# Kernel tuning notes

Measured on AMD Instinct MI355X. Metric: run time of the kernel, lower is better.

The kernel has to match this reference:

```python
import jax, jax.numpy as jnp
import numpy as np

ITER_STEPS = 2
NODE_DIM = 512

def _rmv(t, m, value):
    # allennlp.replace_masked_values: keep t where mask nonzero, else value
    return jnp.where(m != 0, t, value)

def setup_inputs() -> dict:
    key = jax.random.key(0)
    ks = jax.random.split(key, 24)
    B, R, C, D, d = 16, 64, 64, 2048, NODE_DIM
    inp = {
        "question_node": jax.random.normal(ks[0], (B, d), jnp.float32),
        "table_row_header_nodes": jax.random.normal(ks[1], (B, R, d), jnp.float32),
        "table_col_header_nodes": jax.random.normal(ks[2], (B, C, d), jnp.float32),
        "table_data_cell_nodes": jax.random.normal(ks[3], (B, D, d), jnp.float32),
        "table_row_header_index_mask": jax.random.randint(ks[4], (B, R), 0, 2, jnp.int32),
        "table_col_header_index_mask": jax.random.randint(ks[5], (B, C), 0, 2, jnp.int32),
        "table_data_cell_index_mask": jax.random.randint(ks[6], (B, D), 0, 2, jnp.int32),
        "same_row_data_cell_relation": jax.random.randint(ks[7], (B, D, D), 0, 2, jnp.int32),
        "same_col_data_cell_relation": jax.random.randint(ks[8], (B, D, D), 0, 2, jnp.int32),
        "data_cell_row_rel": jax.random.randint(ks[9], (B, R, D), 0, 2, jnp.int32),
        "data_cell_col_rel": jax.random.randint(ks[10], (B, C, D), 0, 2, jnp.int32),
        # parameters (Linear(in,out) stores weight [out,in]; y = x @ W.T)
        "w_node": jax.random.normal(ks[11], (1, d), jnp.float32) / np.sqrt(d),
        "w_row_data_cell": jax.random.normal(ks[12], (d, d), jnp.float32) / np.sqrt(d),
        "w_col_data_cell": jax.random.normal(ks[13], (d, d), jnp.float32) / np.sqrt(d),
        "w_data_cell_row": jax.random.normal(ks[14], (d, d), jnp.float32) / np.sqrt(d),
        "w_data_cell_col": jax.random.normal(ks[15], (d, d), jnp.float32) / np.sqrt(d),
        "w_same_row": jax.random.normal(ks[16], (d, d), jnp.float32) / np.sqrt(d),
        "w_same_col": jax.random.normal(ks[17], (d, d), jnp.float32) / np.sqrt(d),
        "w_row_question": jax.random.normal(ks[18], (d, d), jnp.float32) / np.sqrt(d),
        "w_col_question": jax.random.normal(ks[19], (d, d), jnp.float32) / np.sqrt(d),
    }
    return inp


def reference(question_node, table_row_header_nodes, table_col_header_nodes,
              table_data_cell_nodes, table_row_header_index_mask,
              table_col_header_index_mask, table_data_cell_index_mask,
              same_row_data_cell_relation, same_col_data_cell_relation,
              data_cell_row_rel, data_cell_col_rel,
              w_node, w_row_data_cell, w_col_data_cell, w_data_cell_row,
              w_data_cell_col, w_same_row, w_same_col, w_row_question,
              w_col_question):
    rm = table_row_header_index_mask.astype(jnp.float32)   # [B,R]
    cm = table_col_header_index_mask.astype(jnp.float32)   # [B,C]
    dm = table_data_cell_index_mask.astype(jnp.float32)    # [B,D]

    # masked relation graphs (0/1 float)
    rh_dc_graph = data_cell_row_rel.astype(jnp.float32) * (rm[:, :, None] * dm[:, None, :])   # [B,R,D]
    ch_dc_graph = data_cell_col_rel.astype(jnp.float32) * (cm[:, :, None] * dm[:, None, :])   # [B,C,D]
    dc_dc_mask = dm[:, :, None] * dm[:, None, :]
    same_row_graph = same_row_data_cell_relation.astype(jnp.float32) * dc_dc_mask             # [B,D,D]
    same_col_graph = same_col_data_cell_relation.astype(jnp.float32) * dc_dc_mask             # [B,D,D]

    rh_num = rh_dc_graph.sum(-1)                                  # [B,R]
    rh_num = _rmv(rh_num + 1.0, (rh_num >= 1), 1.0)
    ch_num = ch_dc_graph.sum(-1)                                  # [B,C]
    ch_num = _rmv(ch_num + 1.0, (ch_num >= 1), 1.0)
    dc_num = (same_row_graph.sum(-1) + same_col_graph.sum(-1)
              + rh_dc_graph.sum(1) + ch_dc_graph.sum(1))          # [B,D]
    dc_num = _rmv(dc_num, (dc_num >= 1), 1.0)

    rh = table_row_header_nodes
    ch = table_col_header_nodes
    dc = table_data_cell_nodes
    q = question_node

    for _ in range(ITER_STEPS):
        rh_w = jax.nn.sigmoid(rh @ w_node.T)[..., 0]   # [B,R]
        ch_w = jax.nn.sigmoid(ch @ w_node.T)[..., 0]   # [B,C]
        dc_w = jax.nn.sigmoid(dc @ w_node.T)[..., 0]   # [B,D]

        rh_dc_info = dc @ w_row_data_cell.T            # [B,D,d]
        ch_dc_info = dc @ w_col_data_cell.T            # [B,D,d]
        rh_q_info = (q @ w_row_question.T)[:, None, :] * rm[:, :, None]  # [B,R,d]
        ch_q_info = (q @ w_col_question.T)[:, None, :] * cm[:, :, None]  # [B,C,d]
        same_row_info = dc @ w_same_row.T              # [B,D,d]
        same_col_info = dc @ w_same_col.T              # [B,D,d]
        dc_rh_info = rh @ w_data_cell_row.T            # [B,R,d]
        dc_ch_info = ch @ w_data_cell_col.T            # [B,C,d]

        # gated adjacency weights: source-node sigmoid gate masked by graph
        rh_dc_weight = jnp.where(rh_dc_graph != 0, dc_w[:, None, :], 0.0)         # [B,R,D]
        ch_dc_weight = jnp.where(ch_dc_graph != 0, dc_w[:, None, :], 0.0)         # [B,C,D]
        same_row_weight = jnp.where(same_row_graph != 0, dc_w[:, None, :], 0.0)   # [B,D,D]
        same_col_weight = jnp.where(same_col_graph != 0, dc_w[:, None, :], 0.0)   # [B,D,D]
        dc_rh_weight = jnp.where(jnp.swapaxes(rh_dc_graph, 1, 2) != 0, rh_w[:, None, :], 0.0)  # [B,D,R]
        dc_ch_weight = jnp.where(jnp.swapaxes(ch_dc_graph, 1, 2) != 0, ch_w[:, None, :], 0.0)  # [B,D,C]

        rh_dc_agg = jnp.matmul(rh_dc_weight, rh_dc_info)        # [B,R,d]
        ch_dc_agg = jnp.matmul(ch_dc_weight, ch_dc_info)        # [B,C,d]
        same_row_agg = jnp.matmul(same_row_weight, same_row_info)  # [B,D,d]
        same_col_agg = jnp.matmul(same_col_weight, same_col_info)  # [B,D,d]
        dc_rh_agg = jnp.matmul(dc_rh_weight, dc_rh_info)        # [B,D,d]
        dc_ch_agg = jnp.matmul(dc_ch_weight, dc_ch_info)        # [B,D,d]

        agg_rh = (rh_dc_agg + rh_q_info) / rh_num[:, :, None]
        agg_ch = (ch_dc_agg + ch_q_info) / ch_num[:, :, None]
        # NOTE: faithful to source bug: dc_ch_agg appears twice, same_col_agg unused
        agg_dc = (same_row_agg + dc_ch_agg + dc_rh_agg + dc_ch_agg) / dc_num[:, :, None]

        rh = jax.nn.relu(agg_rh)
        ch = jax.nn.relu(agg_ch)
        dc = jax.nn.relu(agg_dc)

    return (rh, ch, dc)
```

## Files before the change

kernel.cpp:

```cpp
#include <hip/hip_runtime.h>
#include <math.h>

#define NB 16
#define NR 64
#define NCOL 64
#define ND 2048
#define DIM 512

typedef __attribute__((ext_vector_type(4))) float f32x4;
typedef __attribute__((ext_vector_type(8))) short bf16x8;
typedef __attribute__((ext_vector_type(8))) unsigned short us8;

#define OFF_RHNUM  0L
#define OFF_CHNUM  1024L
#define OFF_DCNUM  2048L
#define OFF_RHW    34816L
#define OFF_CHW    35840L
#define OFF_QROW   36864L
#define OFF_QCOL   45056L
#define OFF_PRER   53248L
#define OFF_PREC   577536L
#define OFF_INFORC 1101824L
#define OFF_BITS   2150400L
#define OFF_DCS    4247552L
#define OFF_PROJ   21024768L
#define WS_FLOATS  37801984L

__device__ inline void bsplit(float v, unsigned short& h, unsigned short& l) {
    unsigned uv = __float_as_uint(v);
    unsigned hb = (uv + 0x7FFFu + ((uv >> 16) & 1u)) >> 16;
    h = (unsigned short)hb;
    float lo = v - __uint_as_float(hb << 16);
    unsigned lv = __float_as_uint(lo);
    l = (unsigned short)((lv + 0x7FFFu + ((lv >> 16) & 1u)) >> 16);
}

__device__ inline unsigned spread4(unsigned x) {
    x = (x | (x << 12)) & 0x000F000Fu;
    x = (x | (x << 6))  & 0x03030303u;
    x = (x | (x << 3))  & 0x11111111u;
    return x;
}

__global__ __launch_bounds__(256) void k_gate_rc(
    const float* __restrict__ rh, const float* __restrict__ ch,
    const int* __restrict__ rm, const int* __restrict__ cm,
    const float* __restrict__ wnode,
    float* __restrict__ rh_w, float* __restrict__ ch_w)
{
    int wave = threadIdx.x >> 6, lane = threadIdx.x & 63;
    int idx = blockIdx.x * 4 + wave;
    const float* xrow; float* outw; int mval;
    if (idx < NB * NR) {
        int b = idx >> 6, r = idx & 63;
        xrow = rh + ((long)b * NR + r) * DIM; mval = rm[b * NR + r]; outw = rh_w + b * NR + r;
    } else {
        int tt = idx - NB * NR; int b = tt >> 6, c = tt & 63;
        xrow = ch + ((long)b * NCOL + c) * DIM; mval = cm[b * NCOL + c]; outw = ch_w + b * NCOL + c;
    }
    const float4* px = (const float4*)xrow;
    const float4* pw = (const float4*)wnode;
    float4 xa = px[lane * 2], xb = px[lane * 2 + 1];
    float4 wa = pw[lane * 2], wb = pw[lane * 2 + 1];
    float s = xa.x * wa.x + xa.y * wa.y + xa.z * wa.z + xa.w * wa.w
            + xb.x * wb.x + xb.y * wb.y + xb.z * wb.z + xb.w * wb.w;
    #pragma unroll
    for (int o = 32; o > 0; o >>= 1) s += __shfl_xor(s, o, 64);
    if (lane == 0) {
        float g = 1.f / (1.f + expf(-s));
        *outw = mval ? g : 0.f;
    }
}

__global__ __launch_bounds__(256) void k_split(
    const float* __restrict__ src, const float* __restrict__ wnode, const int* __restrict__ dmask,
    unsigned short* __restrict__ dhi, unsigned short* __restrict__ dlo,
    unsigned short* __restrict__ thi, unsigned short* __restrict__ tlo)
{
    int b = blockIdx.y, j0 = blockIdx.x * 16;
    __shared__ float X[16 * 512];
    __shared__ float scs[16];
    int t = threadIdx.x;
    int r = t >> 4, u = t & 15;
    const float* row = src + ((long)b * ND + j0 + r) * DIM;
    float part = 0.f;
    #pragma unroll
    for (int i = 0; i < 8; i++) {
        int col = i * 64 + u * 4;
        float4 v = *(const float4*)(row + col);
        float4 w = *(const float4*)(wnode + col);
        part += v.x * w.x + v.y * w.y + v.z * w.z + v.w * w.w;
        *(float4*)&X[r * 512 + (col ^ ((r & 7) * 4))] = v;
    }
    part += __shfl_xor(part, 1, 64);
    part += __shfl_xor(part, 2, 64);
    part += __shfl_xor(part, 4, 64);
    part += __shfl_xor(part, 8, 64);
    if (u == 0) {
        float g = 1.f / (1.f + expf(-part));
        scs[r] = (dmask[(long)b * ND + j0 + r] != 0) ? g : 0.f;
    }
    __syncthreads();
    {
        float s = scs[r];
        long ob = ((long)b * ND + j0 + r) * DIM + u * 32;
        #pragma unroll
        for (int g = 0; g < 4; g++) {
            us8 ph, pl;
            #pragma unroll
            for (int e = 0; e < 8; e++) {
                int cc = u * 32 + g * 8 + e;
                float v = X[r * 512 + (cc ^ ((r & 7) * 4))] * s;
                unsigned short hh, ll; bsplit(v, hh, ll);
                ph[e] = hh; pl[e] = ll;
            }
            *(us8*)(dhi + ob + g * 8) = ph;
            *(us8*)(dlo + ob + g * 8) = pl;
        }
    }
    #pragma unroll
    for (int h = 0; h < 2; h++) {
        int n = t + h * 256;
        us8 ph0, ph1, pl0, pl1;
        #pragma unroll
        for (int rr = 0; rr < 16; rr++) {
            float v = X[rr * 512 + (n ^ ((rr & 7) * 4))] * scs[rr];
            unsigned short hh, ll; bsplit(v, hh, ll);
            if (rr < 8) { ph0[rr] = hh; pl0[rr] = ll; }
            else        { ph1[rr - 8] = hh; pl1[rr - 8] = ll; }
        }
        long ob = ((long)b * DIM + n) * ND + j0;
        *(us8*)(thi + ob) = ph0; *(us8*)(thi + ob + 8) = ph1;
        *(us8*)(tlo + ob) = pl0; *(us8*)(tlo + ob + 8) = pl1;
    }
}

__global__ __launch_bounds__(256) void k_wsplit(
    const float* __restrict__ w, unsigned short* __restrict__ whi, unsigned short* __restrict__ wlo)
{
    long i = ((long)blockIdx.x * 256 + threadIdx.x) * 8;
    float4 a = *(const float4*)(w + i), b4 = *(const float4*)(w + i + 4);
    float v[8] = {a.x, a.y, a.z, a.w, b4.x, b4.y, b4.z, b4.w};
    us8 ph, pl;
    #pragma unroll
    for (int t = 0; t < 8; t++) {
        unsigned short hh, ll; bsplit(v[t], hh, ll);
        ph[t] = hh; pl[t] = ll;
    }
    *(us8*)(whi + i) = ph;
    *(us8*)(wlo + i) = pl;
}

__global__ __launch_bounds__(256) void k_q(
    const float* __restrict__ q, const float* __restrict__ wrq, const float* __restrict__ wcq,
    float* __restrict__ qrow, float* __restrict__ qcol)
{
    int b = blockIdx.z;
    const float* W = blockIdx.y ? wcq : wrq;
    float* out = blockIdx.y ? qcol : qrow;
    int wave = threadIdx.x >> 6, lane = threadIdx.x & 63;
    int n = blockIdx.x * 4 + wave;
    const float4* qp = (const float4*)(q + (long)b * DIM);
    const float4* wp = (const float4*)(W + (long)n * DIM);
    float4 a0 = qp[lane * 2], a1 = qp[lane * 2 + 1];
    float4 w0 = wp[lane * 2], w1 = wp[lane * 2 + 1];
    float s = a0.x * w0.x + a0.y * w0.y + a0.z * w0.z + a0.w * w0.w
            + a1.x * w1.x + a1.y * w1.y + a1.z * w1.z + a1.w * w1.w;
    #pragma unroll
    for (int o = 32; o > 0; o >>= 1) s += __shfl_xor(s, o, 64);
    if (lane == 0) out[(long)b * DIM + n] = s;
}

__global__ __launch_bounds__(256) void k_bits(
    const int* __restrict__ sr, const int* __restrict__ sc, const int* __restrict__ dmask,
    unsigned* __restrict__ bits, float* __restrict__ dcnum)
{
    long bi = blockIdx.x;
    int b = (int)(bi >> 11);
    int dmi = dmask[bi];
    int wave = threadIdx.x >> 6, lane = threadIdx.x & 63;
    const int4* sr4 = (const int4*)(sr + bi * ND);
    const int4* sc4 = (const int4*)(sc + bi * ND);
    const int4* dm4 = (const int4*)(dmask + (long)b * ND);
    unsigned* brow = bits + bi * 64;
    int cnt = 0;
    #pragma unroll
    for (int h = 0; h < 2; h++) {
        int vidx = wave * 128 + h * 64 + lane;
        int4 vs = sr4[vidx];
        int4 vc = sc4[vidx];
        int4 vd = dm4[vidx];
        bool d0 = dmi && vd.x, d1 = dmi && vd.y, d2 = dmi && vd.z, d3 = dmi && vd.w;
        unsigned long long m0 = __ballot(d0 && vs.x);
        unsigned long long m1 = __ballot(d1 && vs.y);
        unsigned long long m2 = __ballot(d2 && vs.z);
        unsigned long long m3 = __ballot(d3 && vs.w);
        unsigned long long n0 = __ballot(d0 && vc.x);
        unsigned long long n1 = __ballot(d1 && vc.y);
        unsigned long long n2 = __ballot(d2 && vc.z);
        unsigned long long n3 = __ballot(d3 && vc.w);
        cnt += __popcll(m0) + __popcll(m1) + __popcll(m2) + __popcll(m3)
             + __popcll(n0) + __popcll(n1) + __popcll(n2) + __popcll(n3);
        if (lane < 8) {
            unsigned w = spread4((unsigned)(m0 >> (8 * lane)) & 0xFFu)
                       | (spread4((unsigned)(m1 >> (8 * lane)) & 0xFFu) << 1)
                       | (spread4((unsigned)(m2 >> (8 * lane)) & 0xFFu) << 2)
                       | (spread4((unsigned)(m3 >> (8 * lane)) & 0xFFu) << 3);
            brow[wave * 16 + h * 8 + lane] = w;
        }
    }
    __shared__ int red[4];
    if (lane == 0) red[wave] = cnt;
    __syncthreads();
    if (threadIdx.x == 0) dcnum[bi] = (float)(red[0] + red[1] + red[2] + red[3]);
}

__global__ __launch_bounds__(256) void k_rcnum(
    const int* __restrict__ rel_rd, const int* __restrict__ rel_cd,
    const int* __restrict__ rm, const int* __restrict__ cm, const int* __restrict__ dmask,
    float* __restrict__ rh_num, float* __restrict__ ch_num)
{
    int wave = threadIdx.x >> 6, lane = threadIdx.x & 63;
    long idx = (long)blockIdx.x * 4 + wave;
    const int* row; int mval; float* out; const int* dmb;
    if (idx < NB * NR) {
        int b = (int)(idx >> 6), r = (int)(idx & 63);
        row = rel_rd + ((long)b * NR + r) * ND; mval = rm[b * NR + r];
        out = rh_num + b * NR + r; dmb = dmask + (long)b * ND;
    } else {
        long tt = idx - NB * NR; int b = (int)(tt >> 6), c = (int)(tt & 63);
        row = rel_cd + ((long)b * NCOL + c) * ND; mval = cm[b * NCOL + c];
        out = ch_num + b * NCOL + c; dmb = dmask + (long)b * ND;
    }
    int cnt = 0;
    for (int rr = 0; rr < 32; rr++) {
        int j = rr * 64 + lane;
        cnt += (row[j] != 0 && dmb[j] != 0) ? 1 : 0;
    }
    #pragma unroll
    for (int o = 32; o > 0; o >>= 1) cnt += __shfl_xor(cnt, o, 64);
    if (lane == 0) {
        float s = mval ? (float)cnt : 0.f;
        *out = (s >= 1.f) ? (s + 1.f) : 1.f;
    }
}

__global__ __launch_bounds__(256) void k_dcnum_final(
    const int* __restrict__ rel_rd, const int* __restrict__ rel_cd,
    const int* __restrict__ rm, const int* __restrict__ cm, const int* __restrict__ dmask,
    float* __restrict__ dcnum)
{
    int b = blockIdx.y;
    int j = blockIdx.x * 256 + threadIdx.x;
    const int* rd = rel_rd + (long)b * NR * ND;
    const int* cd = rel_cd + (long)b * NCOL * ND;
    const int* rmb = rm + b * NR;
    const int* cmb = cm + b * NCOL;
    int cnt = 0;
    for (int r = 0; r < NR; r++)  cnt += (rd[(long)r * ND + j] != 0 && rmb[r] != 0) ? 1 : 0;
    for (int c = 0; c < NCOL; c++) cnt += (cd[(long)c * ND + j] != 0 && cmb[c] != 0) ? 1 : 0;
    float add = (dmask[(long)b * ND + j] != 0) ? (float)cnt : 0.f;
    float tv = dcnum[(long)b * ND + j] + add;
    dcnum[(long)b * ND + j] = (tv >= 1.f) ? tv : 1.f;
}

template<int EPI>
__global__ __launch_bounds__(256) void gemm_small(
    const float* __restrict__ A, long sA,
    const float* __restrict__ W,
    float* __restrict__ C, long sC,
    const float* __restrict__ rowscale, float alpha,
    const int* __restrict__ mrow, const float* __restrict__ addvec,
    const float* __restrict__ rownum, int rsb)
{
    int b = blockIdx.z;
    int n0 = blockIdx.x * 64;
    __shared__ float As[32][68], Ws[32][68];
    float acc[4][4] = {};
    int tx = threadIdx.x & 15, ty = threadIdx.x >> 4;
    int lm = threadIdx.x >> 2, lk = (threadIdx.x & 3) * 8;
    const float* Ab = A + (long)b * sA;
    for (int k0 = 0; k0 < DIM; k0 += 32) {
        const float4* pa = (const float4*)(Ab + (long)lm * DIM + k0 + lk);
        float4 va0 = pa[0], va1 = pa[1];
        const float4* pw = (const float4*)(W + (long)(n0 + lm) * DIM + k0 + lk);
        float4 vw0 = pw[0], vw1 = pw[1];
        As[lk + 0][lm] = va0.x; As[lk + 1][lm] = va0.y; As[lk + 2][lm] = va0.z; As[lk + 3][lm] = va0.w;
        As[lk + 4][lm] = va1.x; As[lk + 5][lm] = va1.y; As[lk + 6][lm] = va1.z; As[lk + 7][lm] = va1.w;
        Ws[lk + 0][lm] = vw0.x; Ws[lk + 1][lm] = vw0.y; Ws[lk + 2][lm] = vw0.z; Ws[lk + 3][lm] = vw0.w;
        Ws[lk + 4][lm] = vw1.x; Ws[lk + 5][lm] = vw1.y; Ws[lk + 6][lm] = vw1.z; Ws[lk + 7][lm] = vw1.w;
        __syncthreads();
        #pragma unroll
        for (int kk = 0; kk < 32; kk++) {
            float4 av = *(const float4*)&As[kk][ty * 4];
            float4 wv = *(const float4*)&Ws[kk][tx * 4];
            float a[4] = {av.x, av.y, av.z, av.w};
            float w[4] = {wv.x, wv.y, wv.z, wv.w};
            #pragma unroll
            for (int mi = 0; mi < 4; mi++)
                #pragma unroll
                for (int ni = 0; ni < 4; ni++)
                    acc[mi][ni] += a[mi] * w[ni];
        }
        __syncthreads();
    }
    #pragma unroll
    for (int mi = 0; mi < 4; mi++) {
        int gm = ty * 4 + mi;
        float vals[4];
        if (EPI == 1) {
            float scv = alpha * rowscale[(long)b * rsb + gm];
            #pragma unroll
            for (int ni = 0; ni < 4; ni++) vals[ni] = scv * acc[mi][ni];
        } else {
            float mq = (mrow[(long)b * rsb + gm] != 0) ? 1.f : 0.f;
            float inv = 1.f / rownum[(long)b * rsb + gm];
            #pragma unroll
            for (int ni = 0; ni < 4; ni++) {
                float tv = (acc[mi][ni] + mq * addvec[(long)b * DIM + n0 + tx * 4 + ni]) * inv;
                vals[ni] = fmaxf(tv, 0.f);
            }
        }
        float4 o; o.x = vals[0]; o.y = vals[1]; o.z = vals[2]; o.w = vals[3];
        *(float4*)(C + (long)b * sC + (long)gm * DIM + n0 + tx * 4) = o;
    }
}

__global__ __launch_bounds__(256) void k_pre_rc_mfma(
    const int* __restrict__ rel_rd, const int* __restrict__ rel_cd,
    const unsigned short* __restrict__ thi, const unsigned short* __restrict__ tlo,
    const int* __restrict__ rm, const int* __restrict__ cm,
    float* __restrict__ pre_r, float* __restrict__ pre_c)
{
    int b = blockIdx.y, n0 = blockIdx.x * 64;
    __shared__ unsigned short Aexp[128 * 64];
    __shared__ unsigned short Bhi[64 * 64], Blo[64 * 64];
    int tid = threadIdx.x, lane = tid & 63, wid = tid >> 6;
    int wm = wid >> 1, wn = wid & 1;
    int arow = tid >> 1, aseg = tid & 1;
    const int* relrow = (arow < 64)
        ? rel_rd + ((long)b * 64 + arow) * ND
        : rel_cd + ((long)b * 64 + arow - 64) * ND;
    int bn = tid >> 2, bq = tid & 3;
    const unsigned short* bsrc_h = thi + ((long)b * DIM + n0 + bn) * ND;
    const unsigned short* bsrc_l = tlo + ((long)b * DIM + n0 + bn) * ND;

    f32x4 acc[4][2];
    #pragma unroll
    for (int i = 0; i < 4; i++)
        #pragma unroll
        for (int j = 0; j < 2; j++)
            acc[i][j] = (f32x4){0.f, 0.f, 0.f, 0.f};

    for (int k0 = 0; k0 < ND; k0 += 64) {
        {
            const int4* pa = (const int4*)(relrow + k0 + aseg * 32);
            #pragma unroll
            for (int p = 0; p < 4; p++) {
                int4 v0 = pa[2 * p], v1 = pa[2 * p + 1];
                uint4 qv;
                qv.x = (v0.x ? 0x3F80u : 0u) | (v0.y ? 0x3F800000u : 0u);
                qv.y = (v0.z ? 0x3F80u : 0u) | (v0.w ? 0x3F800000u : 0u);
                qv.z = (v1.x ? 0x3F80u : 0u) | (v1.y ? 0x3F800000u : 0u);
                qv.w = (v1.z ? 0x3F80u : 0u) | (v1.w ? 0x3F800000u : 0u);
                int c = (aseg * 4 + p) ^ (arow & 7);
                *(uint4*)((char*)Aexp + arow * 128 + c * 16) = qv;
            }
        }
        {
            const uint4* ph = (const uint4*)(bsrc_h + k0 + bq * 16);
            const uint4* pl = (const uint4*)(bsrc_l + k0 + bq * 16);
            #pragma unroll
            for (int s = 0; s < 2; s++) {
                int c = (bq * 2 + s) ^ (bn & 7);
                *(uint4*)((char*)Bhi + bn * 128 + c * 16) = ph[s];
                *(uint4*)((char*)Blo + bn * 128 + c * 16) = pl[s];
            }
        }
        __syncthreads();
        #pragma unroll
        for (int ks = 0; ks < 2; ks++) {
            bf16x8 af[4], bh[2], bl[2];
            #pragma unroll
            for (int i = 0; i < 4; i++) {
                int rr = wm * 64 + i * 16 + (lane & 15);
                int cc = (ks * 4 + (lane >> 4)) ^ (rr & 7);
                af[i] = *(bf16x8*)((char*)Aexp + rr * 128 + cc * 16);
            }
            #pragma unroll
            for (int i = 0; i < 2; i++) {
                int nn = wn * 32 + i * 16 + (lane & 15);
                int c2 = (ks * 4 + (lane >> 4)) ^ (nn & 7);
                bh[i] = *(bf16x8*)((char*)Bhi + nn * 128 + c2 * 16);
                bl[i] = *(bf16x8*)((char*)Blo + nn * 128 + c2 * 16);
            }
            #pragma unroll
            for (int mi = 0; mi < 4; mi++)
                #pragma unroll
                for (int ni = 0; ni < 2; ni++) {
                    acc[mi][ni] = __builtin_amdgcn_mfma_f32_16x16x32_bf16(af[mi], bh[ni], acc[mi][ni], 0, 0, 0);
                    acc[mi][ni] = __builtin_amdgcn_mfma_f32_16x16x32_bf16(af[mi], bl[ni], acc[mi][ni], 0, 0, 0);
                }
        }
        __syncthreads();
    }
    const int* msk = wm ? cm : rm;
    float* outp = wm ? pre_c : pre_r;
    #pragma unroll
    for (int mi = 0; mi < 4; mi++) {
        int grow = mi * 16 + (lane >> 4) * 4;
        #pragma unroll
        for (int ni = 0; ni < 2; ni++) {
            int gcol = n0 + wn * 32 + ni * 16 + (lane & 15);
            #pragma unroll
            for (int r = 0; r < 4; r++) {
                int rrow = grow + r;
                float scv = (msk[b * 64 + rrow] != 0) ? 1.f : 0.f;
                outp[((long)b * 64 + rrow) * DIM + gcol] = scv * acc[mi][ni][r];
            }
        }
    }
}

__global__ __launch_bounds__(256) void k_proj_mfma(
    const unsigned short* __restrict__ whi, const unsigned short* __restrict__ wlo,
    const unsigned short* __restrict__ dhi, const unsigned short* __restrict__ dlo,
    unsigned short* __restrict__ phi, unsigned short* __restrict__ plo)
{
    int flat = blockIdx.x;
    int tile = (flat & 7) * 128 + (flat >> 3);
    int b = tile >> 6;
    int rem = tile & 63;
    int m0 = (rem >> 4) * 128;
    int n0 = (rem & 15) * 128;

    __shared__ unsigned short Ahi[128 * 64], Alo[128 * 64];
    __shared__ unsigned short Bhi[128 * 64], Blo[128 * 64];

    int tid = threadIdx.x;
    int lane = tid & 63, wid = tid >> 6;
    int wm = wid >> 1, wn = wid & 1;

    int srow = tid >> 1, sseg = tid & 1;

    f32x4 acc[4][4];
    #pragma unroll
    for (int i = 0; i < 4; i++)
        #pragma unroll
        for (int j = 0; j < 4; j++)
            acc[i][j] = (f32x4){0.f, 0.f, 0.f, 0.f};

    for (int k0 = 0; k0 < DIM; k0 += 64) {
        {
            const uint4* ph = (const uint4*)(whi + (long)(m0 + srow) * DIM + k0 + sseg * 32);
            const uint4* pl = (const uint4*)(wlo + (long)(m0 + srow) * DIM + k0 + sseg * 32);
            #pragma unroll
            for (int s = 0; s < 4; s++) {
                int c = (sseg * 4 + s) ^ (srow & 7);
                *(uint4*)((char*)Ahi + srow * 128 + c * 16) = ph[s];
                *(uint4*)((char*)Alo + srow * 128 + c * 16) = pl[s];
            }
        }
        {
            const uint4* ph = (const uint4*)(dhi + ((long)b * ND + n0 + srow) * DIM + k0 + sseg * 32);
            const uint4* pl = (const uint4*)(dlo + ((long)b * ND + n0 + srow) * DIM + k0 + sseg * 32);
            #pragma unroll
            for (int s = 0; s < 4; s++) {
                int c = (sseg * 4 + s) ^ (srow & 7);
                *(uint4*)((char*)Bhi + srow * 128 + c * 16) = ph[s];
                *(uint4*)((char*)Blo + srow * 128 + c * 16) = pl[s];
            }
        }
        __syncthreads();
        #pragma unroll
        for (int ks = 0; ks < 2; ks++) {
            bf16x8 ah[4], al[4], bh[4], bl[4];
            #pragma unroll
            for (int i = 0; i < 4; i++) {
                int rr = wm * 64 + i * 16 + (lane & 15);
                int cc = (ks * 4 + (lane >> 4)) ^ (rr & 7);
                ah[i] = *(bf16x8*)((char*)Ahi + rr * 128 + cc * 16);
                al[i] = *(bf16x8*)((char*)Alo + rr * 128 + cc * 16);
                int nn = wn * 64 + i * 16 + (lane & 15);
                int c2 = (ks * 4 + (lane >> 4)) ^ (nn & 7);
                bh[i] = *(bf16x8*)((char*)Bhi + nn * 128 + c2 * 16);
                bl[i] = *(bf16x8*)((char*)Blo + nn * 128 + c2 * 16);
            }
            #pragma unroll
            for (int mi = 0; mi < 4; mi++)
                #pragma unroll
                for (int ni = 0; ni < 4; ni++) {
                    acc[mi][ni] = __builtin_amdgcn_mfma_f32_16x16x32_bf16(ah[mi], bh[ni], acc[mi][ni], 0, 0, 0);
                    acc[mi][ni] = __builtin_amdgcn_mfma_f32_16x16x32_bf16(ah[mi], bl[ni], acc[mi][ni], 0, 0, 0);
                    acc[mi][ni] = __builtin_amdgcn_mfma_f32_16x16x32_bf16(al[mi], bh[ni], acc[mi][ni], 0, 0, 0);
                }
        }
        __syncthreads();
    }
    #pragma unroll
    for (int mi = 0; mi < 4; mi++) {
        int grow = m0 + wm * 64 + mi * 16 + (lane >> 4) * 4;
        #pragma unroll
        for (int ni = 0; ni < 4; ni++) {
            int gcol = n0 + wn * 64 + ni * 16 + (lane & 15);
            #pragma unroll
            for (int r = 0; r < 4; r++) {
                unsigned short hh, ll; bsplit(acc[mi][ni][r], hh, ll);
                long off = ((long)b * DIM + grow + r) * ND + gcol;
                phi[off] = hh; plo[off] = ll;
            }
        }
    }
}

__global__ __launch_bounds__(256) void k_aggdc(
    const int* __restrict__ rel_rd, const int* __restrict__ rel_cd,
    const float* __restrict__ info_rc, const int* __restrict__ dmask,
    float* __restrict__ out)
{
    int b = blockIdx.z, m0 = blockIdx.y * 128, n0 = blockIdx.x * 128;
    __shared__ float As[32][132], Bs[32][132];
    float acc[8][8] = {};
    int tx = threadIdx.x & 15, ty = threadIdx.x >> 4;
    int ak = threadIdx.x >> 3, aj = (threadIdx.x & 7) * 16;
    for (int kt = 0; kt < 4; kt++) {
        const int* rel = (kt < 2) ? rel_rd : rel_cd;
        int krow = (kt & 1) * 32 + ak;
        const int4* pa = (const int4*)(rel + ((long)b * 64 + krow) * ND + m0 + aj);
        #pragma unroll
        for (int s = 0; s < 4; s++) {
            int4 v = pa[s];
            float4 f; f.x = v.x ? 1.f : 0.f; f.y = v.y ? 1.f : 0.f; f.z = v.z ? 1.f : 0.f; f.w = v.w ? 1.f : 0.f;
            *(float4*)&As[ak][aj + s * 4] = f;
        }
        const float4* pb = (const float4*)(info_rc + ((long)b * 128 + kt * 32 + ak) * DIM + n0 + aj);
        #pragma unroll
        for (int s = 0; s < 4; s++) *(float4*)&Bs[ak][aj + s * 4] = pb[s];
        __syncthreads();
        #pragma unroll 4
        for (int kk = 0; kk < 32; kk++) {
            float4 a0 = *(const float4*)&As[kk][ty * 8];
            float4 a1 = *(const float4*)&As[kk][ty * 8 + 4];
            float4 b0 = *(const float4*)&Bs[kk][tx * 8];
            float4 b1 = *(const float4*)&Bs[kk][tx * 8 + 4];
            float a[8] = {a0.x, a0.y, a0.z, a0.w, a1.x, a1.y, a1.z, a1.w};
            float w[8] = {b0.x, b0.y, b0.z, b0.w, b1.x, b1.y, b1.z, b1.w};
            #pragma unroll
            for (int mi = 0; mi < 8; mi++)
                #pragma unroll
                for (int ni = 0; ni < 8; ni++)
                    acc[mi][ni] += a[mi] * w[ni];
        }
        __syncthreads();
    }
    #pragma unroll
    for (int mi = 0; mi < 8; mi++) {
        int gm = m0 + ty * 8 + mi;
        float mq = (dmask[(long)b * ND + gm] != 0) ? 1.f : 0.f;
        float* po = out + ((long)b * ND + gm) * DIM + n0 + tx * 8;
        float4 o0; o0.x = mq * acc[mi][0]; o0.y = mq * acc[mi][1]; o0.z = mq * acc[mi][2]; o0.w = mq * acc[mi][3];
        float4 o1; o1.x = mq * acc[mi][4]; o1.y = mq * acc[mi][5]; o1.z = mq * acc[mi][6]; o1.w = mq * acc[mi][7];
        *(float4*)(po) = o0; *(float4*)(po + 4) = o1;
    }
}

__global__ __launch_bounds__(256) void k_agg_final(
    const unsigned* __restrict__ bits,
    const unsigned short* __restrict__ phi, const unsigned short* __restrict__ plo,
    const float* __restrict__ aggdc, const float* __restrict__ rownum,
    float* __restrict__ out)
{
    int flat = blockIdx.x;
    int tile = (flat & 7) * 128 + (flat >> 3);
    int b = tile >> 6;
    int m0 = ((tile >> 2) & 15) * 128;
    int n0 = (tile & 3) * 128;

    __shared__ unsigned short Aexp[128 * 64];
    __shared__ unsigned short Bhi[128 * 64];
    __shared__ unsigned short Blo[128 * 64];

    int tid = threadIdx.x;
    int lane = tid & 63, wid = tid >> 6;
    int wm = wid >> 1, wn = wid & 1;

    int arow = tid >> 1, awsel = tid & 1;
    const unsigned* abit_base = bits + ((long)b * ND + m0 + arow) * 64 + awsel;

    f32x4 acc[4][4];
    #pragma unroll
    for (int i = 0; i < 4; i++)
        #pragma unroll
        for (int j = 0; j < 4; j++)
            acc[i][j] = (f32x4){0.f, 0.f, 0.f, 0.f};

    for (int k0 = 0; k0 < ND; k0 += 64) {
        #pragma unroll
        for (int u = 0; u < 8; u++) {
            int lin = (u & 3) * 256 + tid;
            int n = lin >> 3, c = lin & 7;
            const unsigned short* src = (u < 4 ? phi : plo)
                + ((long)b * DIM + n0 + n) * ND + k0 + c * 8;
            uint4 v = *(const uint4*)src;
            char* dst = (char*)(u < 4 ? Bhi : Blo) + n * 128 + ((c ^ (n & 7)) * 16);
            *(uint4*)dst = v;
        }
        {
            unsigned w = abit_base[k0 >> 5];
            char* ab = (char*)Aexp + arow * 128;
            #pragma unroll
            for (int c = 0; c < 4; c++) {
                uint4 qv;
                qv.x = (((w >> (c * 8 + 0)) & 1u) ? 0x3F80u : 0u) | (((w >> (c * 8 + 1)) & 1u) ? 0x3F800000u : 0u);
                qv.y = (((w >> (c * 8 + 2)) & 1u) ? 0x3F80u : 0u) | (((w >> (c * 8 + 3)) & 1u) ? 0x3F800000u : 0u);
                qv.z = (((w >> (c * 8 + 4)) & 1u) ? 0x3F80u : 0u) | (((w >> (c * 8 + 5)) & 1u) ? 0x3F800000u : 0u);
                qv.w = (((w >> (c * 8 + 6)) & 1u) ? 0x3F80u : 0u) | (((w >> (c * 8 + 7)) & 1u) ? 0x3F800000u : 0u);
                int chunk = (awsel * 4 + c) ^ (arow & 7);
                *(uint4*)(ab + chunk * 16) = qv;
            }
        }
        __syncthreads();
        #pragma unroll
        for (int ks = 0; ks < 2; ks++) {
            bf16x8 af[4], bh[4], bl[4];
            #pragma unroll
            for (int i = 0; i < 4; i++) {
                int rr = wm * 64 + i * 16 + (lane & 15);
                int cc = (ks * 4 + (lane >> 4)) ^ (rr & 7);
                af[i] = *(bf16x8*)((char*)Aexp + rr * 128 + cc * 16);
                int nn = wn * 64 + i * 16 + (lane & 15);
                int c2 = (ks * 4 + (lane >> 4)) ^ (nn & 7);
                bh[i] = *(bf16x8*)((char*)Bhi + nn * 128 + c2 * 16);
                bl[i] = *(bf16x8*)((char*)Blo + nn * 128 + c2 * 16);
            }
            #pragma unroll
            for (int mi = 0; mi < 4; mi++)
                #pragma unroll
                for (int ni = 0; ni < 4; ni++) {
                    acc[mi][ni] = __builtin_amdgcn_mfma_f32_16x16x32_bf16(af[mi], bh[ni], acc[mi][ni], 0, 0, 0);
                    acc[mi][ni] = __builtin_amdgcn_mfma_f32_16x16x32_bf16(af[mi], bl[ni], acc[mi][ni], 0, 0, 0);
                }
        }
        __syncthreads();
    }
    #pragma unroll
    for (int mi = 0; mi < 4; mi++) {
        int grow = m0 + wm * 64 + mi * 16 + (lane >> 4) * 4;
        float inv[4];
        #pragma unroll
        for (int r = 0; r < 4; r++) inv[r] = 1.f / rownum[(long)b * ND + grow + r];
        #pragma unroll
        for (int ni = 0; ni < 4; ni++) {
            int gcol = n0 + wn * 64 + ni * 16 + (lane & 15);
            #pragma unroll
            for (int r = 0; r < 4; r++) {
                long off = ((long)b * ND + grow + r) * DIM + gcol;
                out[off] = fmaxf((acc[mi][ni][r] + aggdc[off]) * inv[r], 0.f);
            }
        }
    }
}

extern "C" void kernel_launch(void* const* d_in, const int* in_sizes, int n_in,
                              void* d_out, int out_size, void* d_ws, size_t ws_size,
                              hipStream_t stream)
{
    const float* q       = (const float*)d_in[0];
    const float* rh0     = (const float*)d_in[1];
    const float* ch0     = (const float*)d_in[2];
    const float* dc0     = (const float*)d_in[3];
    const int*   rm      = (const int*)d_in[4];
    const int*   cm      = (const int*)d_in[5];
    const int*   dmask   = (const int*)d_in[6];
    const int*   same_row= (const int*)d_in[7];
    const int*   same_col= (const int*)d_in[8];
    const int*   rel_rd  = (const int*)d_in[9];
    const int*   rel_cd  = (const int*)d_in[10];
    const float* wnode   = (const float*)d_in[11];
    const float* w_rdc   = (const float*)d_in[12];
    const float* w_cdc   = (const float*)d_in[13];
    const float* w_dcr   = (const float*)d_in[14];
    const float* w_dcc   = (const float*)d_in[15];
    const float* w_sr    = (const float*)d_in[16];
    const float* w_rq    = (const float*)d_in[18];
    const float* w_cq    = (const float*)d_in[19];

    float* out = (float*)d_out;
    float* rh = out;
    float* ch = out + (long)NB * NR * DIM;
    float* dc = out + (long)NB * NR * DIM * 2;

    if (ws_size < (size_t)WS_FLOATS * 4) return;

    float* ws      = (float*)d_ws;
    float* rh_num  = ws + OFF_RHNUM;
    float* ch_num  = ws + OFF_CHNUM;
    float* dc_num  = ws + OFF_DCNUM;
    float* rh_w    = ws + OFF_RHW;
    float* ch_w    = ws + OFF_CHW;
    float* qrow    = ws + OFF_QROW;
    float* qcol    = ws + OFF_QCOL;
    float* pre_r   = ws + OFF_PRER;
    float* pre_c   = ws + OFF_PREC;
    float* info_rc = ws + OFF_INFORC;
    unsigned* bits = (unsigned*)(ws + OFF_BITS);
    unsigned short* dhi = (unsigned short*)(ws + OFF_DCS);
    unsigned short* dlo = dhi + (size_t)NB * ND * DIM;
    unsigned short* thi = (unsigned short*)(ws + OFF_PROJ);
    unsigned short* tlo = thi + (size_t)NB * DIM * ND;
    unsigned short* phi = (unsigned short*)(ws + OFF_PROJ);
    unsigned short* plo = phi + (size_t)NB * DIM * ND;
    float* aggdc   = ws + OFF_DCS;
    unsigned short* whi = (unsigned short*)dc;
    unsigned short* wlo = whi + (size_t)DIM * DIM;

    hipMemcpyAsync(rh, rh0, sizeof(float) * (size_t)NB * NR * DIM, hipMemcpyDeviceToDevice, stream);
    hipMemcpyAsync(ch, ch0, sizeof(float) * (size_t)NB * NCOL * DIM, hipMemcpyDeviceToDevice, stream);

    k_bits<<<NB * ND, 256, 0, stream>>>(same_row, same_col, dmask, bits, dc_num);
    k_rcnum<<<512, 256, 0, stream>>>(rel_rd, rel_cd, rm, cm, dmask, rh_num, ch_num);
    k_dcnum_final<<<dim3(ND / 256, NB), 256, 0, stream>>>(rel_rd, rel_cd, rm, cm, dmask, dc_num);
    k_q<<<dim3(128, 2, NB), 256, 0, stream>>>(q, w_rq, w_cq, qrow, qcol);

    for (int it = 0; it < 2; it++) {
        k_gate_rc<<<512, 256, 0, stream>>>(rh, ch, rm, cm, wnode, rh_w, ch_w);
        k_split<<<dim3(128, NB), 256, 0, stream>>>(it == 0 ? dc0 : dc, wnode, dmask, dhi, dlo, thi, tlo);
        k_wsplit<<<128, 256, 0, stream>>>(w_sr, whi, wlo);
        gemm_small<1><<<dim3(8, 1, NB), 256, 0, stream>>>(rh, (long)NR * DIM, w_dcr,
            info_rc, 128L * DIM, rh_w, 1.0f, nullptr, nullptr, nullptr, NR);
        gemm_small<1><<<dim3(8, 1, NB), 256, 0, stream>>>(ch, (long)NCOL * DIM, w_dcc,
            info_rc + 64L * DIM, 128L * DIM, ch_w, 2.0f, nullptr, nullptr, nullptr, NCOL);
        k_pre_rc_mfma<<<dim3(8, NB), 256, 0, stream>>>(rel_rd, rel_cd, thi, tlo, rm, cm, pre_r, pre_c);
        k_proj_mfma<<<1024, 256, 0, stream>>>(whi, wlo, dhi, dlo, phi, plo);
        k_aggdc<<<dim3(4, 16, NB), 256, 0, stream>>>(rel_rd, rel_cd, info_rc, dmask, aggdc);
        gemm_small<2><<<dim3(8, 1, NB), 256, 0, stream>>>(pre_r, (long)NR * DIM, w_rdc,
            rh, (long)NR * DIM, nullptr, 1.0f, rm, qrow, rh_num, NR);
        gemm_small<2><<<dim3(8, 1, NB), 256, 0, stream>>>(pre_c, (long)NCOL * DIM, w_cdc,
            ch, (long)NCOL * DIM, nullptr, 1.0f, cm, qcol, ch_num, NCOL);
        k_agg_final<<<1024, 256, 0, stream>>>(bits, phi, plo, aggdc, dc_num, dc);
    }
}
```

Before: 1.147 ms.

## Fuse header-to-cell aggregation into final MFMA kernel and register-prefetch GEMM tiles

The separate fp32 k_aggdc GEMM is removed. Its data-cell aggregation over row/col header info is now done as two extra K-steps in k_agg_final. The info GEMM writes transposed bf16 hi/lo splits, and the relation masks are expanded into the A tile inside the final kernel, which removes an fp32 [B,D,d] intermediate write and read plus an extra launch. Both k_proj_mfma and k_agg_final also gain register-staged prefetch of the next K-tile, so global loads overlap with the MFMA work, at the cost of more registers and an extra barrier per step.

Result: slower. 1.769 ms (+54.2%).

```diff
diff --git a/kernel.cpp b/kernel.cpp
--- a/kernel.cpp
+++ b/kernel.cpp
@@ -40,6 +40,33 @@
     x = (x | (x << 6))  & 0x03030303u;
     x = (x | (x << 3))  & 0x11111111u;
     return x;
+}
+
+__device__ inline void mfma_phase2(const unsigned short* Aexp, const unsigned short* Bhi,
+                                   const unsigned short* Blo, int wm, int wn, int lane,
+                                   f32x4 acc[4][4])
+{
+    #pragma unroll
+    for (int ks = 0; ks < 2; ks++) {
+        bf16x8 af[4], bh[4], bl[4];
+        #pragma unroll
+        for (int i = 0; i < 4; i++) {
+            int rr = wm * 64 + i * 16 + (lane & 15);
+            int cc = (ks * 4 + (lane >> 4)) ^ (rr & 7);
+            af[i] = *(const bf16x8*)((const char*)Aexp + rr * 128 + cc * 16);
+            int nn = wn * 64 + i * 16 + (lane & 15);
+            int c2 = (ks * 4 + (lane >> 4)) ^ (nn & 7);
+            bh[i] = *(const bf16x8*)((const char*)Bhi + nn * 128 + c2 * 16);
+            bl[i] = *(const bf16x8*)((const char*)Blo + nn * 128 + c2 * 16);
+        }
+        #pragma unroll
+        for (int mi = 0; mi < 4; mi++)
+            #pragma unroll
+            for (int ni = 0; ni < 4; ni++) {
+                acc[mi][ni] = __builtin_amdgcn_mfma_f32_16x16x32_bf16(af[mi], bh[ni], acc[mi][ni], 0, 0, 0);
+                acc[mi][ni] = __builtin_amdgcn_mfma_f32_16x16x32_bf16(af[mi], bl[ni], acc[mi][ni], 0, 0, 0);
+            }
+    }
 }
 
 __global__ __launch_bounds__(256) void k_gate_rc(
@@ -264,14 +291,11 @@
     dcnum[(long)b * ND + j] = (tv >= 1.f) ? tv : 1.f;
 }
 
-template<int EPI>
-__global__ __launch_bounds__(256) void gemm_small(
+__global__ __launch_bounds__(256) void gemm_info(
     const float* __restrict__ A, long sA,
     const float* __restrict__ W,
-    float* __restrict__ C, long sC,
-    const float* __restrict__ rowscale, float alpha,
-    const int* __restrict__ mrow, const float* __restrict__ addvec,
-    const float* __restrict__ rownum, int rsb)
+    unsigned short* __restrict__ ihiT, unsigned short* __restrict__ iloT, int hoff,
+    const float* __restrict__ rowscale, float alpha)
 {
     int b = blockIdx.z;
     int n0 = blockIdx.x * 64;
@@ -307,21 +331,67 @@
     #pragma unroll
     for (int mi = 0; mi < 4; mi++) {
         int gm = ty * 4 + mi;
-        float vals[4];
-        if (EPI == 1) {
-            float scv = alpha * rowscale[(long)b * rsb + gm];
-            #pragma unroll
-            for (int ni = 0; ni < 4; ni++) vals[ni] = scv * acc[mi][ni];
-        } else {
-            float mq = (mrow[(long)b * rsb + gm] != 0) ? 1.f : 0.f;
-            float inv = 1.f / rownum[(long)b * rsb + gm];
-            #pragma unroll
-            for (int ni = 0; ni < 4; ni++) {
-                float tv = (acc[mi][ni] + mq * addvec[(long)b * DIM + n0 + tx * 4 + ni]) * inv;
-                vals[ni] = fmaxf(tv, 0.f);
-            }
-        }
-        float4 o; o.x = vals[0]; o.y = vals[1]; o.z = vals[2]; o.w = vals[3];
+        float scv = alpha * rowscale[(long)b * 64 + gm];
+        #pragma unroll
+        for (int ni = 0; ni < 4; ni++) {
+            float v = scv * acc[mi][ni];
+            unsigned short hh, ll; bsplit(v, hh, ll);
+            long off = ((long)b * DIM + n0 + tx * 4 + ni) * 128 + hoff + gm;
+            ihiT[off] = hh; iloT[off] = ll;
+        }
+    }
+}
+
+__global__ __launch_bounds__(256) void gemm_head(
+    const float* __restrict__ A, long sA,
+    const float* __restrict__ W,
+    float* __restrict__ C, long sC,
+    const int* __restrict__ mrow, const float* __restrict__ addvec,
+    const float* __restrict__ rownum)
+{
+    int b = blockIdx.z;
+    int n0 = blockIdx.x * 64;
+    __shared__ float As[32][68], Ws[32][68];
+    float acc[4][4] = {};
+    int tx = threadIdx.x & 15, ty = threadIdx.x >> 4;
+    int lm = threadIdx.x >> 2, lk = (threadIdx.x & 3) * 8;
+    const float* Ab = A + (long)b * sA;
+    for (int k0 = 0; k0 < DIM; k0 += 32) {
+        const float4* pa = (const float4*)(Ab + (long)lm * DIM + k0 + lk);
+        float4 va0 = pa[0], va1 = pa[1];
+        const float4* pw = (const float4*)(W + (long)(n0 + lm) * DIM + k0 + lk);
+        float4 vw0 = pw[0], vw1 = pw[1];
+        As[lk + 0][lm] = va0.x; As[lk + 1][lm] = va0.y; As[lk + 2][lm] = va0.z; As[lk + 3][lm] = va0.w;
+        As[lk + 4][lm] = va1.x; As[lk + 5][lm] = va1.y; As[lk + 6][lm] = va1.z; As[lk + 7][lm] = va1.w;
+        Ws[lk + 0][lm] = vw0.x; Ws[lk + 1][lm] = vw0.y; Ws[lk + 2][lm] = vw0.z; Ws[lk + 3][lm] = vw0.w;
+        Ws[lk + 4][lm] = vw1.x; Ws[lk + 5][lm] = vw1.y; Ws[lk + 6][lm] = vw1.z; Ws[lk + 7][lm] = vw1.w;
+        __syncthreads();
+        #pragma unroll
+        for (int kk = 0; kk < 32; kk++) {
+            float4 av = *(const float4*)&As[kk][ty * 4];
+            float4 wv = *(const float4*)&Ws[kk][tx * 4];
+            float a[4] = {av.x, av.y, av.z, av.w};
+            float w[4] = {wv.x, wv.y, wv.z, wv.w};
+            #pragma unroll
+            for (int mi = 0; mi < 4; mi++)
+                #pragma unroll
+                for (int ni = 0; ni < 4; ni++)
+                    acc[mi][ni] += a[mi] * w[ni];
+        }
+        __syncthreads();
+    }
+    #pragma unroll
+    for (int mi = 0; mi < 4; mi++) {
+        int gm = ty * 4 + mi;
+        float mq = (mrow[(long)b * 64 + gm] != 0) ? 1.f : 0.f;
+        float inv = 1.f / rownum[(long)b * 64 + gm];
+        float4 o;
+        float* vo = (float*)&o;
+        #pragma unroll
+        for (int ni = 0; ni < 4; ni++) {
+            float tv = (acc[mi][ni] + mq * addvec[(long)b * DIM + n0 + tx * 4 + ni]) * inv;
+            vo[ni] = fmaxf(tv, 0.f);
+        }
         *(float4*)(C + (long)b * sC + (long)gm * DIM + n0 + tx * 4) = o;
     }
 }
@@ -440,8 +510,34 @@
     int tid = threadIdx.x;
     int lane = tid & 63, wid = tid >> 6;
     int wm = wid >> 1, wn = wid & 1;
-
     int srow = tid >> 1, sseg = tid & 1;
+
+    const unsigned short* sa_h = whi + (long)(m0 + srow) * DIM + sseg * 32;
+    const unsigned short* sa_l = wlo + (long)(m0 + srow) * DIM + sseg * 32;
+    const unsigned short* sb_h = dhi + ((long)b * ND + n0 + srow) * DIM + sseg * 32;
+    const unsigned short* sb_l = dlo + ((long)b * ND + n0 + srow) * DIM + sseg * 32;
+
+    uint4 ra_h[4], ra_l[4], rb_h[4], rb_l[4];
+    auto p_load = [&](int t) {
+        long ko = (long)t * 64;
+        #pragma unroll
+        for (int s = 0; s < 4; s++) {
+            ra_h[s] = *(const uint4*)(sa_h + ko + s * 8);
+            ra_l[s] = *(const uint4*)(sa_l + ko + s * 8);
+            rb_h[s] = *(const uint4*)(sb_h + ko + s * 8);
+            rb_l[s] = *(const uint4*)(sb_l + ko + s * 8);
+        }
+    };
+    auto p_write = [&]() {
+        #pragma unroll
+        for (int s = 0; s < 4; s++) {
+            int c = (sseg * 4 + s) ^ (srow & 7);
+            *(uint4*)((char*)Ahi + srow * 128 + c * 16) = ra_h[s];
+            *(uint4*)((char*)Alo + srow * 128 + c * 16) = ra_l[s];
+            *(uint4*)((char*)Bhi + srow * 128 + c * 16) = rb_h[s];
+            *(uint4*)((char*)Blo + srow * 128 + c * 16) = rb_l[s];
+        }
+    };
 
     f32x4 acc[4][4];
     #pragma unroll
@@ -450,28 +546,11 @@
         for (int j = 0; j < 4; j++)
             acc[i][j] = (f32x4){0.f, 0.f, 0.f, 0.f};
 
-    for (int k0 = 0; k0 < DIM; k0 += 64) {
-        {
-            const uint4* ph = (const uint4*)(whi + (long)(m0 + srow) * DIM + k0 + sseg * 32);
-            const uint4* pl = (const uint4*)(wlo + (long)(m0 + srow) * DIM + k0 + sseg * 32);
-            #pragma unroll
-            for (int s = 0; s < 4; s++) {
-                int c = (sseg * 4 + s) ^ (srow & 7);
-                *(uint4*)((char*)Ahi + srow * 128 + c * 16) = ph[s];
-                *(uint4*)((char*)Alo + srow * 128 + c * 16) = pl[s];
-            }
-        }
-        {
-            const uint4* ph = (const uint4*)(dhi + ((long)b * ND + n0 + srow) * DIM + k0 + sseg * 32);
-            const uint4* pl = (const uint4*)(dlo + ((long)b * ND + n0 + srow) * DIM + k0 + sseg * 32);
-            #pragma unroll
-            for (int s = 0; s < 4; s++) {
-                int c = (sseg * 4 + s) ^ (srow & 7);
-                *(uint4*)((char*)Bhi + srow * 128 + c * 16) = ph[s];
-                *(uint4*)((char*)Blo + srow * 128 + c * 16) = pl[s];
-            }
-        }
-        __syncthreads();
+    p_load(0);
+    p_write();
+    __syncthreads();
+    for (int t = 0; t < 8; t++) {
+        if (t < 7) p_load(t + 1);
         #pragma unroll
         for (int ks = 0; ks < 2; ks++) {
             bf16x8 ah[4], al[4], bh[4], bl[4];
@@ -496,6 +575,7 @@
                 }
         }
         __syncthreads();
+        if (t < 7) { p_write(); __syncthreads(); }
     }
     #pragma unroll
     for (int mi = 0; mi < 4; mi++) {
@@ -513,61 +593,12 @@
     }
 }
 
-__global__ __launch_bounds__(256) void k_aggdc(
-    const int* __restrict__ rel_rd, const int* __restrict__ rel_cd,
-    const float* __restrict__ info_rc, const int* __restrict__ dmask,
-    float* __restrict__ out)
-{
-    int b = blockIdx.z, m0 = blockIdx.y * 128, n0 = blockIdx.x * 128;
-    __shared__ float As[32][132], Bs[32][132];
-    float acc[8][8] = {};
-    int tx = threadIdx.x & 15, ty = threadIdx.x >> 4;
-    int ak = threadIdx.x >> 3, aj = (threadIdx.x & 7) * 16;
-    for (int kt = 0; kt < 4; kt++) {
-        const int* rel = (kt < 2) ? rel_rd : rel_cd;
-        int krow = (kt & 1) * 32 + ak;
-        const int4* pa = (const int4*)(rel + ((long)b * 64 + krow) * ND + m0 + aj);
-        #pragma unroll
-        for (int s = 0; s < 4; s++) {
-            int4 v = pa[s];
-            float4 f; f.x = v.x ? 1.f : 0.f; f.y = v.y ? 1.f : 0.f; f.z = v.z ? 1.f : 0.f; f.w = v.w ? 1.f : 0.f;
-            *(float4*)&As[ak][aj + s * 4] = f;
-        }
-        const float4* pb = (const float4*)(info_rc + ((long)b * 128 + kt * 32 + ak) * DIM + n0 + aj);
-        #pragma unroll
-        for (int s = 0; s < 4; s++) *(float4*)&Bs[ak][aj + s * 4] = pb[s];
-        __syncthreads();
-        #pragma unroll 4
-        for (int kk = 0; kk < 32; kk++) {
-            float4 a0 = *(const float4*)&As[kk][ty * 8];
-            float4 a1 = *(const float4*)&As[kk][ty * 8 + 4];
-            float4 b0 = *(const float4*)&Bs[kk][tx * 8];
-            float4 b1 = *(const float4*)&Bs[kk][tx * 8 + 4];
-            float a[8] = {a0.x, a0.y, a0.z, a0.w, a1.x, a1.y, a1.z, a1.w};
-            float w[8] = {b0.x, b0.y, b0.z, b0.w, b1.x, b1.y, b1.z, b1.w};
-            #pragma unroll
-            for (int mi = 0; mi < 8; mi++)
-                #pragma unroll
-                for (int ni = 0; ni < 8; ni++)
-                    acc[mi][ni] += a[mi] * w[ni];
-        }
-        __syncthreads();
-    }
-    #pragma unroll
-    for (int mi = 0; mi < 8; mi++) {
-        int gm = m0 + ty * 8 + mi;
-        float mq = (dmask[(long)b * ND + gm] != 0) ? 1.f : 0.f;
-        float* po = out + ((long)b * ND + gm) * DIM + n0 + tx * 8;
-        float4 o0; o0.x = mq * acc[mi][0]; o0.y = mq * acc[mi][1]; o0.z = mq * acc[mi][2]; o0.w = mq * acc[mi][3];
-        float4 o1; o1.x = mq * acc[mi][4]; o1.y = mq * acc[mi][5]; o1.z = mq * acc[mi][6]; o1.w = mq * acc[mi][7];
-        *(float4*)(po) = o0; *(float4*)(po + 4) = o1;
-    }
-}
-
 __global__ __launch_bounds__(256) void k_agg_final(
     const unsigned* __restrict__ bits,
     const unsigned short* __restrict__ phi, const unsigned short* __restrict__ plo,
-    const float* __restrict__ aggdc, const float* __restrict__ rownum,
+    const unsigned short* __restrict__ ihiT, const unsigned short* __restrict__ iloT,
+    const int* __restrict__ rel_rd, const int* __restrict__ rel_cd,
+    const int* __restrict__ dmask, const float* __restrict__ rownum,
     float* __restrict__ out)
 {
     int flat = blockIdx.x;
@@ -579,13 +610,52 @@
     __shared__ unsigned short Aexp[128 * 64];
     __shared__ unsigned short Bhi[128 * 64];
     __shared__ unsigned short Blo[128 * 64];
+    __shared__ unsigned short dmu[128];
 
     int tid = threadIdx.x;
     int lane = tid & 63, wid = tid >> 6;
     int wm = wid >> 1, wn = wid & 1;
 
+    if (tid < 128) dmu[tid] = (dmask[(long)b * ND + m0 + tid] != 0) ? 0x3F80 : 0;
+
+    const unsigned short* bsrc[8];
+    char* bdst[8];
+    int bn_[8], bc_[8];
+    #pragma unroll
+    for (int u = 0; u < 8; u++) {
+        int lin = (u & 3) * 256 + tid;
+        int n = lin >> 3, c = lin & 7;
+        bn_[u] = n; bc_[u] = c;
+        bsrc[u] = (u < 4 ? phi : plo) + ((long)b * DIM + n0 + n) * ND + c * 8;
+        bdst[u] = (char*)(u < 4 ? Bhi : Blo) + n * 128 + ((c ^ (n & 7)) * 16);
+    }
     int arow = tid >> 1, awsel = tid & 1;
     const unsigned* abit_base = bits + ((long)b * ND + m0 + arow) * 64 + awsel;
+    char* adst = (char*)Aexp + arow * 128;
+
+    uint4 rb[8];
+    unsigned raw;
+    auto b_load = [&](int t) {
+        long ko = (long)t * 64;
+        #pragma unroll
+        for (int u = 0; u < 8; u++) rb[u] = *(const uint4*)(bsrc[u] + ko);
+        raw = abit_base[t * 2];
+    };
+    auto stage_write = [&]() {
+        #pragma unroll
+        for (int u = 0; u < 8; u++) *(uint4*)(bdst[u]) = rb[u];
+        unsigned w = raw;
+        #pragma unroll
+        for (int c = 0; c < 4; c++) {
+            uint4 qv;
+            qv.x = (((w >> (c * 8 + 0)) & 1u) ? 0x3F80u : 0u) | (((w >> (c * 8 + 1)) & 1u) ? 0x3F800000u : 0u);
+            qv.y = (((w >> (c * 8 + 2)) & 1u) ? 0x3F80u : 0u) | (((w >> (c * 8 + 3)) & 1u) ? 0x3F800000u : 0u);
+            qv.z = (((w >> (c * 8 + 4)) & 1u) ? 0x3F80u : 0u) | (((w >> (c * 8 + 5)) & 1u) ? 0x3F800000u : 0u);
+            qv.w = (((w >> (c * 8 + 6)) & 1u) ? 0x3F80u : 0u) | (((w >> (c * 8 + 7)) & 1u) ? 0x3F800000u : 0u);
+            int chunk = (awsel * 4 + c) ^ (arow & 7);
+            *(uint4*)(adst + chunk * 16) = qv;
+        }
+    };
 
     f32x4 acc[4][4];
     #pragma unroll
@@ -594,53 +664,42 @@
         for (int j = 0; j < 4; j++)
             acc[i][j] = (f32x4){0.f, 0.f, 0.f, 0.f};
 
-    for (int k0 = 0; k0 < ND; k0 += 64) {
+    b_load(0);
+    stage_write();
+    __syncthreads();
+    for (int t = 0; t < 32; t++) {
+        if (t < 31) b_load(t + 1);
+        mfma_phase2(Aexp, Bhi, Blo, wm, wn, lane, acc);
+        __syncthreads();
+        if (t < 31) { stage_write(); __syncthreads(); }
+    }
+    #pragma unroll
+    for (int kt = 0; kt < 2; kt++) {
         #pragma unroll
         for (int u = 0; u < 8; u++) {
-            int lin = (u & 3) * 256 + tid;
-            int n = lin >> 3, c = lin & 7;
-            const unsigned short* src = (u < 4 ? phi : plo)
-                + ((long)b * DIM + n0 + n) * ND + k0 + c * 8;
-            uint4 v = *(const uint4*)src;
-            char* dst = (char*)(u < 4 ? Bhi : Blo) + n * 128 + ((c ^ (n & 7)) * 16);
-            *(uint4*)dst = v;
-        }
-        {
-            unsigned w = abit_base[k0 >> 5];
-            char* ab = (char*)Aexp + arow * 128;
-            #pragma unroll
-            for (int c = 0; c < 4; c++) {
-                uint4 qv;
-                qv.x = (((w >> (c * 8 + 0)) & 1u) ? 0x3F80u : 0u) | (((w >> (c * 8 + 1)) & 1u) ? 0x3F800000u : 0u);
-                qv.y = (((w >> (c * 8 + 2)) & 1u) ? 0x3F80u : 0u) | (((w >> (c * 8 + 3)) & 1u) ? 0x3F800000u : 0u);
-                qv.z = (((w >> (c * 8 + 4)) & 1u) ? 0x3F80u : 0u) | (((w >> (c * 8 + 5)) & 1u) ? 0x3F800000u : 0u);
-                qv.w = (((w >> (c * 8 + 6)) & 1u) ? 0x3F80u : 0u) | (((w >> (c * 8 + 7)) & 1u) ? 0x3F800000u : 0u);
-                int chunk = (awsel * 4 + c) ^ (arow & 7);
-                *(uint4*)(ab + chunk * 16) = qv;
-            }
-        }
-        __syncthreads();
-        #pragma unroll
-        for (int ks = 0; ks < 2; ks++) {
-            bf16x8 af[4], bh[4], bl[4];
-            #pragma unroll
-            for (int i = 0; i < 4; i++) {
-                int rr = wm * 64 + i * 16 + (lane & 15);
-                int cc = (ks * 4 + (lane >> 4)) ^ (rr & 7);
-                af[i] = *(bf16x8*)((char*)Aexp + rr * 128 + cc * 16);
-                int nn = wn * 64 + i * 16 + (lane & 15);
-                int c2 = (ks * 4 + (lane >> 4)) ^ (nn & 7);
-                bh[i] = *(bf16x8*)((char*)Bhi + nn * 128 + c2 * 16);
-                bl[i] = *(bf16x8*)((char*)Blo + nn * 128 + c2 * 16);
-            }
-            #pragma unroll
-            for (int mi = 0; mi < 4; mi++)
-                #pragma unroll
-                for (int ni = 0; ni < 4; ni++) {
-                    acc[mi][ni] = __builtin_amdgcn_mfma_f32_16x16x32_bf16(af[mi], bh[ni], acc[mi][ni], 0, 0, 0);
-                    acc[mi][ni] = __builtin_amdgcn_mfma_f32_16x16x32_bf16(af[mi], bl[ni], acc[mi][ni], 0, 0, 0);
-                }
-        }
+            uint4 v = *(const uint4*)((u < 4 ? ihiT : iloT)
+                + ((long)b * DIM + n0 + bn_[u]) * 128 + kt * 64 + bc_[u] * 8);
+            *(uint4*)(bdst[u]) = v;
+        }
+        const int* rel = kt ? rel_cd : rel_rd;
+        #pragma unroll
+        for (int p = 0; p < 8; p++) {
+            int lin = p * 256 + tid;
+            int h = lin >> 5, q = lin & 31;
+            int4 v = *(const int4*)(rel + ((long)b * 64 + h) * ND + m0 + q * 4);
+            int cell = q * 4;
+            unsigned short e0 = v.x ? dmu[cell + 0] : (unsigned short)0;
+            unsigned short e1 = v.y ? dmu[cell + 1] : (unsigned short)0;
+            unsigned short e2 = v.z ? dmu[cell + 2] : (unsigned short)0;
+            unsigned short e3 = v.w ? dmu[cell + 3] : (unsigned short)0;
+            int hc = h >> 3, he = h & 7;
+            *(unsigned short*)((char*)Aexp + (cell + 0) * 128 + ((hc ^ ((cell + 0) & 7)) * 16) + he * 2) = e0;
+            *(unsigned short*)((char*)Aexp + (cell + 1) * 128 + ((hc ^ ((cell + 1) & 7)) * 16) + he * 2) = e1;
+            *(unsigned short*)((char*)Aexp + (cell + 2) * 128 + ((hc ^ ((cell + 2) & 7)) * 16) + he * 2) = e2;
+            *(unsigned short*)((char*)Aexp + (cell + 3) * 128 + ((hc ^ ((cell + 3) & 7)) * 16) + he * 2) = e3;
+        }
+        __syncthreads();
+        mfma_phase2(Aexp, Bhi, Blo, wm, wn, lane, acc);
         __syncthreads();
     }
     #pragma unroll
@@ -655,7 +714,7 @@
             #pragma unroll
             for (int r = 0; r < 4; r++) {
                 long off = ((long)b * ND + grow + r) * DIM + gcol;
-                out[off] = fmaxf((acc[mi][ni][r] + aggdc[off]) * inv[r], 0.f);
+                out[off] = fmaxf(acc[mi][ni][r] * inv[r], 0.f);
             }
         }
     }
@@ -702,7 +761,8 @@
     float* qcol    = ws + OFF_QCOL;
     float* pre_r   = ws + OFF_PRER;
     float* pre_c   = ws + OFF_PREC;
-    float* info_rc = ws + OFF_INFORC;
+    unsigned short* ihiT = (unsigned short*)(ws + OFF_INFORC);
+    unsigned short* iloT = ihiT + (size_t)NB * DIM * 128;
     unsigned* bits = (unsigned*)(ws + OFF_BITS);
     unsigned short* dhi = (unsigned short*)(ws + OFF_DCS);
     unsigned short* dlo = dhi + (size_t)NB * ND * DIM;
@@ -710,7 +770,6 @@
     unsigned short* tlo = thi + (size_t)NB * DIM * ND;
     unsigned short* phi = (unsigned short*)(ws + OFF_PROJ);
     unsigned short* plo = phi + (size_t)NB * DIM * ND;
-    float* aggdc   = ws + OFF_DCS;
     unsigned short* whi = (unsigned short*)dc;
     unsigned short* wlo = whi + (size_t)DIM * DIM;
 
@@ -726,17 +785,17 @@
         k_gate_rc<<<512, 256, 0, stream>>>(rh, ch, rm, cm, wnode, rh_w, ch_w);
         k_split<<<dim3(128, NB), 256, 0, stream>>>(it == 0 ? dc0 : dc, wnode, dmask, dhi, dlo, thi, tlo);
         k_wsplit<<<128, 256, 0, stream>>>(w_sr, whi, wlo);
-        gemm_small<1><<<dim3(8, 1, NB), 256, 0, stream>>>(rh, (long)NR * DIM, w_dcr,
-            info_rc, 128L * DIM, rh_w, 1.0f, nullptr, nullptr, nullptr, NR);
-        gemm_small<1><<<dim3(8, 1, NB), 256, 0, stream>>>(ch, (long)NCOL * DIM, w_dcc,
-            info_rc + 64L * DIM, 128L * DIM, ch_w, 2.0f, nullptr, nullptr, nullptr, NCOL);
+        gemm_info<<<dim3(8, 1, NB), 256, 0, stream>>>(rh, (long)NR * DIM, w_dcr,
+            ihiT, iloT, 0, rh_w, 1.0f);
+        gemm_info<<<dim3(8, 1, NB), 256, 0, stream>>>(ch, (long)NCOL * DIM, w_dcc,
+            ihiT, iloT, 64, ch_w, 2.0f);
         k_pre_rc_mfma<<<dim3(8, NB), 256, 0, stream>>>(rel_rd, rel_cd, thi, tlo, rm, cm, pre_r, pre_c);
         k_proj_mfma<<<1024, 256, 0, stream>>>(whi, wlo, dhi, dlo, phi, plo);
-        k_aggdc<<<dim3(4, 16, NB), 256, 0, stream>>>(rel_rd, rel_cd, info_rc, dmask, aggdc);
-        gemm_small<2><<<dim3(8, 1, NB), 256, 0, stream>>>(pre_r, (long)NR * DIM, w_rdc,
-            rh, (long)NR * DIM, nullptr, 1.0f, rm, qrow, rh_num, NR);
-        gemm_small<2><<<dim3(8, 1, NB), 256, 0, stream>>>(pre_c, (long)NCOL * DIM, w_cdc,
-            ch, (long)NCOL * DIM, nullptr, 1.0f, cm, qcol, ch_num, NCOL);
-        k_agg_final<<<1024, 256, 0, stream>>>(bits, phi, plo, aggdc, dc_num, dc);
-    }
-}
+        gemm_head<<<dim3(8, 1, NB), 256, 0, stream>>>(pre_r, (long)NR * DIM, w_rdc,
+            rh, (long)NR * DIM, rm, qrow, rh_num);
+        gemm_head<<<dim3(8, 1, NB), 256, 0, stream>>>(pre_c, (long)NCOL * DIM, w_cdc,
+            ch, (long)NCOL * DIM, cm, qcol, ch_num);
+        k_agg_final<<<1024, 256, 0, stream>>>(bits, phi, plo, ihiT, iloT,
+            rel_rd, rel_cd, dmask, dc_num, dc);
+    }
+}
```
